# Performance work log

Hardware: AMD Instinct MI355X
Metric: run time of the kernel (lower is better)

## Reference

```python
import jax, jax.numpy as jnp
import numpy as np

N = 100000      # nodes
E = 1600000     # edges (avg degree 16)
F_IN = 300      # input feature dim
H = 64          # hidden channels
OUT = 20        # output classes
L = 8           # num GCN2Conv layers
ALPHA = 0.1
THETA = 0.5


def setup_inputs() -> dict:
    key = jax.random.key(0)
    ks = jax.random.split(key, 6)
    x = jax.random.normal(ks[0], (N, F_IN), jnp.float32)
    edge_index = jax.random.randint(ks[1], (2, E), 0, N, dtype=jnp.int32)
    edge_weights = jax.random.uniform(ks[2], (E,), jnp.float32)
    W_in = jax.random.normal(ks[3], (F_IN, H), jnp.float32) / np.sqrt(F_IN)
    b_in = jnp.zeros((H,), jnp.float32)
    conv_w = jax.random.normal(ks[4], (L, H, H), jnp.float32) / np.sqrt(H)
    W_out = jax.random.normal(ks[5], (H, OUT), jnp.float32) / np.sqrt(H)
    b_out = jnp.zeros((OUT,), jnp.float32)
    return dict(x=x, edge_index=edge_index, edge_weights=edge_weights,
                W_in=W_in, b_in=b_in, conv_w=conv_w, W_out=W_out, b_out=b_out)


def _gcn_norm(edge_index, edge_weights, n, dtype):
    # add self-loops with weight 1, symmetric normalization (PyG gcn_norm)
    loop = jnp.arange(n, dtype=edge_index.dtype)
    row = jnp.concatenate([edge_index[0], loop])
    col = jnp.concatenate([edge_index[1], loop])
    w = jnp.concatenate([edge_weights, jnp.ones((n,), dtype)])
    deg = jax.ops.segment_sum(w, col, num_segments=n)
    dinv = jnp.where(deg > 0, jax.lax.rsqrt(deg), 0.0).astype(dtype)
    norm = dinv[row] * w * dinv[col]
    return row, col, norm


def reference(x, edge_index, edge_weights, W_in, b_in, conv_w, W_out, b_out):
    n = x.shape[0]
    row, col, norm = _gcn_norm(edge_index, edge_weights, n, x.dtype)
    # eval mode: dropout is identity
    h = jax.nn.relu(x @ W_in + b_in)   # start_with_lin (F_IN != H)
    x0 = h
    num_layers = conv_w.shape[0]
    for l in range(num_layers):
        beta = float(np.log(THETA / (l + 1) + 1.0))
        # A_hat @ h : gather sources, weight by norm, scatter-add to targets
        agg = jax.ops.segment_sum(norm[:, None] * h[row], col, num_segments=n)
        z = (1.0 - ALPHA) * agg + ALPHA * x0  # initial-residual mixing
        h = jax.nn.relu((1.0 - beta) * z + beta * (z @ conv_w[l]))
    return h @ W_out + b_out
```

## Files before the change

kernel.cpp:

```cpp
#include <hip/hip_runtime.h>
#include <hip/hip_fp16.h>
#include <math.h>


#define HID 64
#define FIN 300
#define NOUT 20
#define ALPHA 0.1f
#define DSCALE 262144.0f
#define CNT_SHIFT 25
#define DEG_MASK 0x1FFFFFFu
#define FBLK 1024

typedef _Float16 f16;
typedef f16 f16x8 __attribute__((ext_vector_type(8)));
typedef float f32x4 __attribute__((ext_vector_type(4)));

__device__ __forceinline__ float wdec(unsigned v) {
    union { unsigned short u; __half h; } c;
    c.u = (unsigned short)(v >> 17);
    return __half2float(c.h);
}

__device__ __forceinline__ void unpack8(const float4& v, float* f) {
    const __half2* p = reinterpret_cast<const __half2*>(&v);
#pragma unroll
    for (int i = 0; i < 4; ++i) {
        float2 t = __half22float2(p[i]);
        f[2 * i] = t.x;
        f[2 * i + 1] = t.y;
    }
}

__global__ void accum_k(const int* __restrict__ row, const int* __restrict__ col,
                        const float* __restrict__ ew,
                        unsigned* __restrict__ packed,
                        uint2* __restrict__ rec, int e) {
    int i = blockIdx.x * blockDim.x + threadIdx.x;
    if (i < e) {
        int c = col[i], r = row[i];
        float wv = ew[i];
        unsigned q = (unsigned)__float2uint_rn(wv * DSCALE);
        unsigned old = atomicAdd(&packed[c], (1u << CNT_SHIFT) | q);
        unsigned rank = (old >> CNT_SHIFT) & 0x7Fu;
        union { __half h; unsigned short u; } cv;
        cv.h = __float2half(wv);
        rec[i] = make_uint2((unsigned)c | (rank << 17),
                            (unsigned)r | ((unsigned)cv.u << 17));
    }
}

__global__ __launch_bounds__(1024) void unpackscan_k(const unsigned* __restrict__ packed,
                                                     float* __restrict__ dinv,
                                                     int* __restrict__ padcnt,
                                                     int* __restrict__ bsum, int n) {
    __shared__ int ws[16];
    int t = threadIdx.x, i = blockIdx.x * 1024 + t;
    int pad = 0;
    if (i < n) {
        unsigned v = packed[i];
        int cnt = (int)(v >> CNT_SHIFT);
        float d = 1.0f + (float)(v & DEG_MASK) * (1.0f / DSCALE);
        dinv[i] = rsqrtf(d);
        pad = (cnt + 3) & ~3;
        padcnt[i] = pad;
    }
    int s = pad;
#pragma unroll
    for (int d = 1; d < 64; d <<= 1) s += __shfl_xor(s, d);
    if ((t & 63) == 0) ws[t >> 6] = s;
    __syncthreads();
    if (t == 0) {
        int tot = 0;
#pragma unroll
        for (int k = 0; k < 16; ++k) tot += ws[k];
        bsum[blockIdx.x] = tot;
    }
}

__global__ void scan2_k(int* __restrict__ bsum, int nb, int* __restrict__ rp, int n) {
    int lane = threadIdx.x;
    int acc = 0;
    for (int base = 0; base < nb; base += 64) {
        int idx = base + lane;
        int orig = (idx < nb) ? bsum[idx] : 0;
        int v = orig;
#pragma unroll
        for (int d = 1; d < 64; d <<= 1) {
            int u = __shfl_up(v, d);
            if (lane >= d) v += u;
        }
        if (idx < nb) bsum[idx] = acc + v - orig;
        acc += __shfl(v, 63);
    }
    if (lane == 0) rp[n] = acc;
}

__global__ __launch_bounds__(1024) void scan3_k(const int* __restrict__ padcnt,
                                                const unsigned* __restrict__ packed,
                                                const int* __restrict__ bsum,
                                                int* __restrict__ rp,
                                                unsigned* __restrict__ edges, int n) {
    __shared__ int ws[16];
    int t = threadIdx.x, i = blockIdx.x * 1024 + t;
    int lane = t & 63, w = t >> 6;
    int v = (i < n) ? padcnt[i] : 0;
    int sv = v;
#pragma unroll
    for (int d = 1; d < 64; d <<= 1) {
        int u = __shfl_up(sv, d);
        if (lane >= d) sv += u;
    }
    if (lane == 63) ws[w] = sv;
    __syncthreads();
    if (w == 0) {
        int x = (lane < 16) ? ws[lane] : 0;
#pragma unroll
        for (int d = 1; d < 16; d <<= 1) {
            int u = __shfl_up(x, d);
            if (lane >= d) x += u;
        }
        if (lane < 16) ws[lane] = x;
    }
    __syncthreads();
    int woff = (w > 0) ? ws[w - 1] : 0;
    if (i < n) {
        int base = bsum[blockIdx.x] + woff + sv - v;
        rp[i] = base;
        int cnt = (int)(packed[i] >> CNT_SHIFT);
        for (int k = cnt; k < v; ++k) edges[base + k] = 0u;
    }
}

__global__ void wt_k(const float* __restrict__ Win, f16* __restrict__ Wt) {
    int i = blockIdx.x * blockDim.x + threadIdx.x;
    if (i < 64 * 320) {
        int c = i / 320, k = i - c * 320;
        Wt[i] = (k < FIN) ? (f16)Win[k * 64 + c] : (f16)0.0f;
    }
}

__global__ __launch_bounds__(256) void fgi_k(const uint2* __restrict__ rec,
                                             const float* __restrict__ dinv,
                                             const int* __restrict__ rp,
                                             unsigned* __restrict__ edges, int e,
                                             const float* __restrict__ x,
                                             const f16* __restrict__ Wt,
                                             const float* __restrict__ bin,
                                             __half* __restrict__ x0h, int n) {
    __shared__ f16 As[64 * 72];
    int t = threadIdx.x;
    if (blockIdx.x < FBLK) {
        int xcd = blockIdx.x & 7;
        int lo = (int)(((long long)n * xcd) >> 3);
        int hi = (int)(((long long)n * (xcd + 1)) >> 3);
        int stride = (FBLK >> 3) * 256;
        for (int i = (blockIdx.x >> 3) * 256 + t; i < e; i += stride) {
            uint2 rc = rec[i];
            int c = (int)(rc.x & 0x1FFFFu);
            if (c < lo || c >= hi) continue;
            int r = (int)(rc.y & 0x1FFFFu);
            union { unsigned short u; __half h; } ev;
            ev.u = (unsigned short)(rc.y >> 17);
            float nw = (1.0f - ALPHA) * dinv[r] * __half2float(ev.h) * dinv[c];
            union { __half h; unsigned short u; } cv;
            cv.h = __float2half(nw);
            int rank = (int)((rc.x >> 17) & 0x7Fu);
            edges[rp[c] + rank] = ((unsigned)cv.u << 17) | (unsigned)r;
        }
        return;
    }
    int lane = t & 63, wv = t >> 6;
    int node0 = (blockIdx.x - FBLK) * 64;
    int lr = lane & 15, kg = lane >> 4;
    int fi = t & 15, rowbase = t >> 4;
    f32x4 acc0 = {0, 0, 0, 0}, acc1 = {0, 0, 0, 0}, acc2 = {0, 0, 0, 0}, acc3 = {0, 0, 0, 0};
    float4 xr[4];
    auto loadchunk = [&](int c) {
#pragma unroll
        for (int it = 0; it < 4; ++it) {
            int rw = rowbase + it * 16;
            int rr = node0 + rw;
            rr = (rr < n) ? rr : (n - 1);
            int kbase = c * 64 + fi * 4;
            xr[it] = make_float4(0.f, 0.f, 0.f, 0.f);
            if (kbase < FIN)
                xr[it] = *reinterpret_cast<const float4*>(x + (size_t)rr * FIN + kbase);
        }
    };
    loadchunk(0);
    for (int c = 0; c < 5; ++c) {
        __syncthreads();
#pragma unroll
        for (int it = 0; it < 4; ++it) {
            int rw = rowbase + it * 16;
            union { float2 f2; f16 h[4]; } u;
            u.h[0] = (f16)xr[it].x; u.h[1] = (f16)xr[it].y;
            u.h[2] = (f16)xr[it].z; u.h[3] = (f16)xr[it].w;
            *reinterpret_cast<float2*>(As + rw * 72 + fi * 4) = u.f2;
        }
        __syncthreads();
        if (c < 4) loadchunk(c + 1);
#pragma unroll
        for (int ks = 0; ks < 2; ++ks) {
            f16x8 a = *(const f16x8*)(As + (wv * 16 + lr) * 72 + ks * 32 + kg * 8);
            const f16* wb = Wt + c * 64 + ks * 32 + kg * 8;
            f16x8 b0 = *(const f16x8*)(wb + (0 * 16 + lr) * 320);
            f16x8 b1 = *(const f16x8*)(wb + (1 * 16 + lr) * 320);
            f16x8 b2 = *(const f16x8*)(wb + (2 * 16 + lr) * 320);
            f16x8 b3 = *(const f16x8*)(wb + (3 * 16 + lr) * 320);
            acc0 = __builtin_amdgcn_mfma_f32_16x16x32_f16(a, b0, acc0, 0, 0, 0);
            acc1 = __builtin_amdgcn_mfma_f32_16x16x32_f16(a, b1, acc1, 0, 0, 0);
            acc2 = __builtin_amdgcn_mfma_f32_16x16x32_f16(a, b2, acc2, 0, 0, 0);
            acc3 = __builtin_amdgcn_mfma_f32_16x16x32_f16(a, b3, acc3, 0, 0, 0);
        }
    }
    float bi0 = bin[0 * 16 + lr], bi1 = bin[1 * 16 + lr];
    float bi2 = bin[2 * 16 + lr], bi3 = bin[3 * 16 + lr];
    f16 ov[4][4];
#pragma unroll
    for (int r = 0; r < 4; ++r) {
        ov[0][r] = (f16)fmaxf(acc0[r] + bi0, 0.f);
        ov[1][r] = (f16)fmaxf(acc1[r] + bi1, 0.f);
        ov[2][r] = (f16)fmaxf(acc2[r] + bi2, 0.f);
        ov[3][r] = (f16)fmaxf(acc3[r] + bi3, 0.f);
    }
    __syncthreads();
#pragma unroll
    for (int cg = 0; cg < 4; ++cg)
#pragma unroll
        for (int r = 0; r < 4; ++r)
            As[(wv * 16 + kg * 4 + r) * 72 + cg * 16 + lr] = ov[cg][r];
    __syncthreads();
#pragma unroll
    for (int it = 0; it < 2; ++it) {
        int idx = t + it * 256;
        int rw = idx >> 3, ch = idx & 7;
        int node = node0 + rw;
        if (node < n)
            ((float4*)(x0h + (size_t)node * 64))[ch] =
                *reinterpret_cast<const float4*>(As + rw * 72 + ch * 8);
    }
}

__global__ __launch_bounds__(256) void layer_k(const int* __restrict__ rp,
                                               const unsigned* __restrict__ edges,
                                               const float* __restrict__ dinv,
                                               const __half* __restrict__ x0h,
                                               const __half* __restrict__ hin,
                                               __half* __restrict__ hout,
                                               const float* __restrict__ Wl,
                                               float beta, int n,
                                               const float* __restrict__ Wout,
                                               const float* __restrict__ bout,
                                               float* __restrict__ out) {
    __shared__ f16 As[64 * 72];
    __shared__ f16 Bs[64 * 72];
    int t = threadIdx.x, lane = t & 63, wv = t >> 6;
    int node0 = blockIdx.x * 64;
    for (int i = t; i < 4096; i += 256) {
        int k = i >> 6, c = i & 63;
        Bs[c * 72 + k] = (f16)Wl[i];
    }
    int g = lane >> 3, c8 = lane & 7;
#pragma unroll
    for (int pass = 0; pass < 2; ++pass) {
        int row = pass * 32 + wv * 8 + g;
        int node = node0 + row;
        int nd = (node < n) ? node : (n - 1);
        int j = rp[nd], end = (node < n) ? rp[nd + 1] : j;
        float a0[8], a1[8], a2[8], a3[8];
#pragma unroll
        for (int i = 0; i < 8; ++i) { a0[i] = 0.f; a1[i] = 0.f; a2[i] = 0.f; a3[i] = 0.f; }
        while (__any(j < end)) {
            if (j < end) {
                uint4 e4 = *reinterpret_cast<const uint4*>(edges + j);
                float w0 = wdec(e4.x), w1 = wdec(e4.y), w2 = wdec(e4.z), w3 = wdec(e4.w);
                float4 r0 = ((const float4*)(hin + (size_t)(e4.x & 0x1FFFF) * 64))[c8];
                float4 r1 = ((const float4*)(hin + (size_t)(e4.y & 0x1FFFF) * 64))[c8];
                float4 r2 = ((const float4*)(hin + (size_t)(e4.z & 0x1FFFF) * 64))[c8];
                float4 r3 = ((const float4*)(hin + (size_t)(e4.w & 0x1FFFF) * 64))[c8];
                float f0[8], f1[8], f2[8], f3[8];
                unpack8(r0, f0);
                unpack8(r1, f1);
                unpack8(r2, f2);
                unpack8(r3, f3);
#pragma unroll
                for (int i = 0; i < 8; ++i) {
                    a0[i] = fmaf(w0, f0[i], a0[i]);
                    a1[i] = fmaf(w1, f1[i], a1[i]);
                    a2[i] = fmaf(w2, f2[i], a2[i]);
                    a3[i] = fmaf(w3, f3[i], a3[i]);
                }
            }
            j += 4;
        }
        float di = dinv[nd];
        float c1 = (1.0f - ALPHA) * di * di;
        float4 hs4 = ((const float4*)(hin + (size_t)nd * 64))[c8];
        float4 xs4 = ((const float4*)(x0h + (size_t)nd * 64))[c8];
        float hf[8], xf[8];
        unpack8(hs4, hf);
        unpack8(xs4, xf);
        f16x8 zv8;
#pragma unroll
        for (int i = 0; i < 8; ++i)
            zv8[i] = (f16)fmaf(ALPHA, xf[i],
                               fmaf(c1, hf[i], (a0[i] + a1[i]) + (a2[i] + a3[i])));
        *(f16x8*)(As + row * 72 + c8 * 8) = zv8;
    }
    __syncthreads();
    int lr = lane & 15, kg = lane >> 4;
    f32x4 acc0 = {0, 0, 0, 0}, acc1 = {0, 0, 0, 0}, acc2 = {0, 0, 0, 0}, acc3 = {0, 0, 0, 0};
    f16x8 af0 = *(const f16x8*)(As + (wv * 16 + lr) * 72 + kg * 8);
    f16x8 af1 = *(const f16x8*)(As + (wv * 16 + lr) * 72 + 32 + kg * 8);
    {
        f16x8 b0 = *(const f16x8*)(Bs + (0 * 16 + lr) * 72 + kg * 8);
        f16x8 b1 = *(const f16x8*)(Bs + (0 * 16 + lr) * 72 + 32 + kg * 8);
        acc0 = __builtin_amdgcn_mfma_f32_16x16x32_f16(af0, b0, acc0, 0, 0, 0);
        acc0 = __builtin_amdgcn_mfma_f32_16x16x32_f16(af1, b1, acc0, 0, 0, 0);
    }
    {
        f16x8 b0 = *(const f16x8*)(Bs + (1 * 16 + lr) * 72 + kg * 8);
        f16x8 b1 = *(const f16x8*)(Bs + (1 * 16 + lr) * 72 + 32 + kg * 8);
        acc1 = __builtin_amdgcn_mfma_f32_16x16x32_f16(af0, b0, acc1, 0, 0, 0);
        acc1 = __builtin_amdgcn_mfma_f32_16x16x32_f16(af1, b1, acc1, 0, 0, 0);
    }
    {
        f16x8 b0 = *(const f16x8*)(Bs + (2 * 16 + lr) * 72 + kg * 8);
        f16x8 b1 = *(const f16x8*)(Bs + (2 * 16 + lr) * 72 + 32 + kg * 8);
        acc2 = __builtin_amdgcn_mfma_f32_16x16x32_f16(af0, b0, acc2, 0, 0, 0);
        acc2 = __builtin_amdgcn_mfma_f32_16x16x32_f16(af1, b1, acc2, 0, 0, 0);
    }
    {
        f16x8 b0 = *(const f16x8*)(Bs + (3 * 16 + lr) * 72 + kg * 8);
        f16x8 b1 = *(const f16x8*)(Bs + (3 * 16 + lr) * 72 + 32 + kg * 8);
        acc3 = __builtin_amdgcn_mfma_f32_16x16x32_f16(af0, b0, acc3, 0, 0, 0);
        acc3 = __builtin_amdgcn_mfma_f32_16x16x32_f16(af1, b1, acc3, 0, 0, 0);
    }
    float omb = 1.0f - beta;
    f16 ov[4][4];
#pragma unroll
    for (int cg = 0; cg < 4; ++cg) {
        f32x4 acc = (cg == 0) ? acc0 : (cg == 1) ? acc1 : (cg == 2) ? acc2 : acc3;
        int col = cg * 16 + lr;
#pragma unroll
        for (int r = 0; r < 4; ++r) {
            float zv = (float)As[(wv * 16 + kg * 4 + r) * 72 + col];
            ov[cg][r] = (f16)fmaxf(fmaf(beta, acc[r], omb * zv), 0.f);
        }
    }
    __syncthreads();
#pragma unroll
    for (int cg = 0; cg < 4; ++cg)
#pragma unroll
        for (int r = 0; r < 4; ++r)
            As[(wv * 16 + kg * 4 + r) * 72 + cg * 16 + lr] = ov[cg][r];
    __syncthreads();

    if (!Wout) {
#pragma unroll
        for (int it = 0; it < 2; ++it) {
            int idx = t + it * 256;
            int rw = idx >> 3, ch = idx & 7;
            int node = node0 + rw;
            if (node < n)
                ((float4*)(hout + (size_t)node * 64))[ch] =
                    *reinterpret_cast<const float4*>(As + rw * 72 + ch * 8);
        }
    } else {
        for (int i = t; i < 32 * 64; i += 256) {
            int c = i >> 6, k = i & 63;
            Bs[c * 72 + k] = (c < NOUT) ? (f16)Wout[k * NOUT + c] : (f16)0.0f;
        }
        __syncthreads();
        f16x8 ha0 = *(const f16x8*)(As + (wv * 16 + lr) * 72 + kg * 8);
        f16x8 ha1 = *(const f16x8*)(As + (wv * 16 + lr) * 72 + 32 + kg * 8);
#pragma unroll
        for (int ct = 0; ct < 2; ++ct) {
            f32x4 oacc = {0, 0, 0, 0};
            f16x8 b0 = *(const f16x8*)(Bs + (ct * 16 + lr) * 72 + kg * 8);
            f16x8 b1 = *(const f16x8*)(Bs + (ct * 16 + lr) * 72 + 32 + kg * 8);
            oacc = __builtin_amdgcn_mfma_f32_16x16x32_f16(ha0, b0, oacc, 0, 0, 0);
            oacc = __builtin_amdgcn_mfma_f32_16x16x32_f16(ha1, b1, oacc, 0, 0, 0);
            int col = ct * 16 + lr;
            if (col < NOUT) {
                float bo = bout[col];
#pragma unroll
                for (int r = 0; r < 4; ++r) {
                    int nd2 = node0 + wv * 16 + kg * 4 + r;
                    if (nd2 < n) out[(size_t)nd2 * NOUT + col] = oacc[r] + bo;
                }
            }
        }
    }
}

extern "C" void kernel_launch(void* const* d_in, const int* in_sizes, int n_in,
                              void* d_out, int out_size, void* d_ws, size_t ws_size,
                              hipStream_t stream) {
    const float* x    = (const float*)d_in[0];
    const int*   ei   = (const int*)d_in[1];
    const float* ew   = (const float*)d_in[2];
    const float* Win  = (const float*)d_in[3];
    const float* bin  = (const float*)d_in[4];
    const float* cw   = (const float*)d_in[5];
    const float* Wout = (const float*)d_in[6];
    const float* bout = (const float*)d_in[7];

    const int n = in_sizes[0] / FIN;
    const int e = in_sizes[2];
    const int L = in_sizes[5] / (HID * HID);
    const int* row = ei;
    const int* col = ei + e;
    const int epadmax = e + 3 * n + 64;

    size_t off = 0;
    auto alloc = [&](size_t bytes) -> char* {
        char* q = (char*)d_ws + off;
        off = (off + bytes + 255) & ~(size_t)255;
        return q;
    };
    __half* x0h  = (__half*)alloc((size_t)n * HID * 2);
    __half* hA   = (__half*)alloc((size_t)n * HID * 2);
    __half* hB   = (__half*)alloc((size_t)n * HID * 2);
    unsigned* edges = (unsigned*)alloc((size_t)epadmax * 4);
    uint2* rec   = (uint2*)alloc((size_t)e * 8);
    unsigned* packed = (unsigned*)alloc((size_t)n * 4);
    float* dinv  = (float*)alloc((size_t)n * 4);
    int*   padcnt= (int*)alloc((size_t)n * 4);
    int*   rp    = (int*)alloc((size_t)(n + 1) * 4);
    int*   bsum  = (int*)alloc(1024 * 4);
    f16*   Wt    = (f16*)alloc((size_t)64 * 320 * 2);

    const int nb = (n + 1023) / 1024;
    const int ntile = (n + 63) / 64;

    hipMemsetAsync(packed, 0, (size_t)n * 4, stream);
    wt_k<<<(64 * 320 + 255) / 256, 256, 0, stream>>>(Win, Wt);
    accum_k<<<(e + 255) / 256, 256, 0, stream>>>(row, col, ew, packed, rec, e);
    unpackscan_k<<<nb, 1024, 0, stream>>>(packed, dinv, padcnt, bsum, n);
    scan2_k<<<1, 64, 0, stream>>>(bsum, nb, rp, n);
    scan3_k<<<nb, 1024, 0, stream>>>(padcnt, packed, bsum, rp, edges, n);

    fgi_k<<<FBLK + ntile, 256, 0, stream>>>(rec, dinv, rp, edges, e,
                                            x, Wt, bin, x0h, n);

    const __half* hin = x0h;
    __half* hout = hA;
    for (int l = 0; l < L; ++l) {
        float beta = (float)log(0.5 / (double)(l + 1) + 1.0);
        bool last = (l == L - 1);
        layer_k<<<ntile, 256, 0, stream>>>(rp, edges, dinv, x0h, hin, hout,
                                           cw + (size_t)l * HID * HID, beta, n,
                                           last ? Wout : nullptr,
                                           last ? bout : nullptr,
                                           last ? (float*)d_out : nullptr);
        hin = hout;
        hout = (hout == hA) ? hB : hA;
    }
}
```

Before: 481.5 us.

## Dynamically assign node rows to 8-lane groups via shared work queue

Replaces the fixed two-pass row assignment in the layer kernel with a dynamic queue: each 8-lane group takes a row, and when it finishes it grabs the next row index from a shared-memory atomic counter. This targets load imbalance from varying node degrees, where a wave used to stall until its longest row finished. In exchange the loop carries extra control flow, a shared atomic and shuffle per iteration, plus an added block barrier.

```diff
diff --git a/kernel.cpp b/kernel.cpp
--- a/kernel.cpp
+++ b/kernel.cpp
@@ -256,58 +256,81 @@
                                                float* __restrict__ out) {
     __shared__ f16 As[64 * 72];
     __shared__ f16 Bs[64 * 72];
+    __shared__ int qctr;
     int t = threadIdx.x, lane = t & 63, wv = t >> 6;
     int node0 = blockIdx.x * 64;
+    if (t == 0) qctr = 32;
     for (int i = t; i < 4096; i += 256) {
         int k = i >> 6, c = i & 63;
         Bs[c * 72 + k] = (f16)Wl[i];
     }
-    int g = lane >> 3, c8 = lane & 7;
-#pragma unroll
-    for (int pass = 0; pass < 2; ++pass) {
-        int row = pass * 32 + wv * 8 + g;
-        int node = node0 + row;
-        int nd = (node < n) ? node : (n - 1);
-        int j = rp[nd], end = (node < n) ? rp[nd + 1] : j;
-        float a0[8], a1[8], a2[8], a3[8];
+    int c8 = lane & 7;
+    __syncthreads();
+
+    int myrow = t >> 3;
+    int nd = 0, j = 0, end = 0;
+    float a0[8], a1[8], a2[8], a3[8];
+    {
+        int node = node0 + myrow;
+        nd = (node < n) ? node : (n - 1);
+        j = rp[nd];
+        end = (node < n) ? rp[nd + 1] : j;
 #pragma unroll
         for (int i = 0; i < 8; ++i) { a0[i] = 0.f; a1[i] = 0.f; a2[i] = 0.f; a3[i] = 0.f; }
-        while (__any(j < end)) {
-            if (j < end) {
-                uint4 e4 = *reinterpret_cast<const uint4*>(edges + j);
-                float w0 = wdec(e4.x), w1 = wdec(e4.y), w2 = wdec(e4.z), w3 = wdec(e4.w);
-                float4 r0 = ((const float4*)(hin + (size_t)(e4.x & 0x1FFFF) * 64))[c8];
-                float4 r1 = ((const float4*)(hin + (size_t)(e4.y & 0x1FFFF) * 64))[c8];
-                float4 r2 = ((const float4*)(hin + (size_t)(e4.z & 0x1FFFF) * 64))[c8];
-                float4 r3 = ((const float4*)(hin + (size_t)(e4.w & 0x1FFFF) * 64))[c8];
-                float f0[8], f1[8], f2[8], f3[8];
-                unpack8(r0, f0);
-                unpack8(r1, f1);
-                unpack8(r2, f2);
-                unpack8(r3, f3);
-#pragma unroll
-                for (int i = 0; i < 8; ++i) {
-                    a0[i] = fmaf(w0, f0[i], a0[i]);
-                    a1[i] = fmaf(w1, f1[i], a1[i]);
-                    a2[i] = fmaf(w2, f2[i], a2[i]);
-                    a3[i] = fmaf(w3, f3[i], a3[i]);
-                }
+    }
+    for (;;) {
+        bool fin = (myrow >= 0) && (j >= end);
+        if (fin) {
+            float di = dinv[nd];
+            float c1 = (1.0f - ALPHA) * di * di;
+            float4 hs4 = ((const float4*)(hin + (size_t)nd * 64))[c8];
+            float4 xs4 = ((const float4*)(x0h + (size_t)nd * 64))[c8];
+            float hf[8], xf[8];
+            unpack8(hs4, hf);
+            unpack8(xs4, xf);
+            f16x8 zv8;
+#pragma unroll
+            for (int i = 0; i < 8; ++i)
+                zv8[i] = (f16)fmaf(ALPHA, xf[i],
+                                   fmaf(c1, hf[i], (a0[i] + a1[i]) + (a2[i] + a3[i])));
+            *(f16x8*)(As + myrow * 72 + c8 * 8) = zv8;
+        }
+        int newrow = 1 << 30;
+        if (fin && c8 == 0) newrow = atomicAdd(&qctr, 1);
+        newrow = __shfl(newrow, lane & 56);
+        if (fin) {
+            myrow = (newrow < 64) ? newrow : -1;
+            if (myrow >= 0) {
+                int node = node0 + myrow;
+                nd = (node < n) ? node : (n - 1);
+                j = rp[nd];
+                end = (node < n) ? rp[nd + 1] : j;
+#pragma unroll
+                for (int i = 0; i < 8; ++i) { a0[i] = 0.f; a1[i] = 0.f; a2[i] = 0.f; a3[i] = 0.f; }
+            }
+        }
+        if (!__any(myrow >= 0)) break;
+        if (myrow >= 0 && j < end) {
+            uint4 e4 = *reinterpret_cast<const uint4*>(edges + j);
+            float w0 = wdec(e4.x), w1 = wdec(e4.y), w2 = wdec(e4.z), w3 = wdec(e4.w);
+            float4 r0 = ((const float4*)(hin + (size_t)(e4.x & 0x1FFFF) * 64))[c8];
+            float4 r1 = ((const float4*)(hin + (size_t)(e4.y & 0x1FFFF) * 64))[c8];
+            float4 r2 = ((const float4*)(hin + (size_t)(e4.z & 0x1FFFF) * 64))[c8];
+            float4 r3 = ((const float4*)(hin + (size_t)(e4.w & 0x1FFFF) * 64))[c8];
+            float f0[8], f1[8], f2[8], f3[8];
+            unpack8(r0, f0);
+            unpack8(r1, f1);
+            unpack8(r2, f2);
+            unpack8(r3, f3);
+#pragma unroll
+            for (int i = 0; i < 8; ++i) {
+                a0[i] = fmaf(w0, f0[i], a0[i]);
+                a1[i] = fmaf(w1, f1[i], a1[i]);
+                a2[i] = fmaf(w2, f2[i], a2[i]);
+                a3[i] = fmaf(w3, f3[i], a3[i]);
             }
             j += 4;
         }
-        float di = dinv[nd];
-        float c1 = (1.0f - ALPHA) * di * di;
-        float4 hs4 = ((const float4*)(hin + (size_t)nd * 64))[c8];
-        float4 xs4 = ((const float4*)(x0h + (size_t)nd * 64))[c8];
-        float hf[8], xf[8];
-        unpack8(hs4, hf);
-        unpack8(xs4, xf);
-        f16x8 zv8;
-#pragma unroll
-        for (int i = 0; i < 8; ++i)
-            zv8[i] = (f16)fmaf(ALPHA, xf[i],
-                               fmaf(c1, hf[i], (a0[i] + a1[i]) + (a2[i] + a3[i])));
-        *(f16x8*)(As + row * 72 + c8 * 8) = zv8;
     }
     __syncthreads();
     int lr = lane & 15, kg = lane >> 4;
```

Result: slower. 543.9 us (+13.0%).

## Split fused edge-fill/input-GEMM kernel and double-buffer input feature loads

Applied to the files above, without the earlier changes.

Splits the combined kernel, where one set of blocks filled the CSR edge array and another set computed the input projection GEMM, into two separate kernels launched back to back. The input GEMM now prefetches two chunks of x ahead using two register buffers, where before it held one. The intent is to stop the edge-fill blocks and the GEMM blocks from competing for the same launch, and to hide more of the global-memory latency of the x reads. In exchange, the two phases can no longer overlap, there is one extra kernel launch, and the GEMM uses more registers.

```diff
diff --git a/kernel.cpp b/kernel.cpp
--- a/kernel.cpp
+++ b/kernel.cpp
@@ -10,7 +10,6 @@
 #define DSCALE 262144.0f
 #define CNT_SHIFT 25
 #define DEG_MASK 0x1FFFFFFu
-#define FBLK 1024
 
 typedef _Float16 f16;
 typedef f16 f16x8 __attribute__((ext_vector_type(8)));
@@ -132,6 +131,31 @@
     }
 }
 
+__global__ __launch_bounds__(256) void fill_k(const uint2* __restrict__ rec,
+                                              const float* __restrict__ dinv,
+                                              const int* __restrict__ rp,
+                                              unsigned* __restrict__ edges,
+                                              int e, int n) {
+    int xcd = blockIdx.x & 7;
+    int lo = (int)(((long long)n * xcd) >> 3);
+    int hi = (int)(((long long)n * (xcd + 1)) >> 3);
+    int nblk = gridDim.x >> 3;
+    int stride = nblk * 256;
+    for (int i = (blockIdx.x >> 3) * 256 + threadIdx.x; i < e; i += stride) {
+        uint2 rc = rec[i];
+        int c = (int)(rc.x & 0x1FFFFu);
+        if (c < lo || c >= hi) continue;
+        int r = (int)(rc.y & 0x1FFFFu);
+        union { unsigned short u; __half h; } ev;
+        ev.u = (unsigned short)(rc.y >> 17);
+        float nw = (1.0f - ALPHA) * dinv[r] * __half2float(ev.h) * dinv[c];
+        union { __half h; unsigned short u; } cv;
+        cv.h = __float2half(nw);
+        int rank = (int)((rc.x >> 17) & 0x7Fu);
+        edges[rp[c] + rank] = ((unsigned)cv.u << 17) | (unsigned)r;
+    }
+}
+
 __global__ void wt_k(const float* __restrict__ Win, f16* __restrict__ Wt) {
     int i = blockIdx.x * blockDim.x + threadIdx.x;
     if (i < 64 * 320) {
@@ -140,81 +164,75 @@
     }
 }
 
-__global__ __launch_bounds__(256) void fgi_k(const uint2* __restrict__ rec,
-                                             const float* __restrict__ dinv,
-                                             const int* __restrict__ rp,
-                                             unsigned* __restrict__ edges, int e,
-                                             const float* __restrict__ x,
-                                             const f16* __restrict__ Wt,
-                                             const float* __restrict__ bin,
-                                             __half* __restrict__ x0h, int n) {
+__global__ __launch_bounds__(256) void gemm_in_k(const float* __restrict__ x,
+                                                 const f16* __restrict__ Wt,
+                                                 const float* __restrict__ bin,
+                                                 __half* __restrict__ x0h, int n) {
     __shared__ f16 As[64 * 72];
-    int t = threadIdx.x;
-    if (blockIdx.x < FBLK) {
-        int xcd = blockIdx.x & 7;
-        int lo = (int)(((long long)n * xcd) >> 3);
-        int hi = (int)(((long long)n * (xcd + 1)) >> 3);
-        int stride = (FBLK >> 3) * 256;
-        for (int i = (blockIdx.x >> 3) * 256 + t; i < e; i += stride) {
-            uint2 rc = rec[i];
-            int c = (int)(rc.x & 0x1FFFFu);
-            if (c < lo || c >= hi) continue;
-            int r = (int)(rc.y & 0x1FFFFu);
-            union { unsigned short u; __half h; } ev;
-            ev.u = (unsigned short)(rc.y >> 17);
-            float nw = (1.0f - ALPHA) * dinv[r] * __half2float(ev.h) * dinv[c];
-            union { __half h; unsigned short u; } cv;
-            cv.h = __float2half(nw);
-            int rank = (int)((rc.x >> 17) & 0x7Fu);
-            edges[rp[c] + rank] = ((unsigned)cv.u << 17) | (unsigned)r;
-        }
-        return;
-    }
-    int lane = t & 63, wv = t >> 6;
-    int node0 = (blockIdx.x - FBLK) * 64;
+    int t = threadIdx.x, lane = t & 63, wv = t >> 6;
+    int node0 = blockIdx.x * 64;
     int lr = lane & 15, kg = lane >> 4;
     int fi = t & 15, rowbase = t >> 4;
     f32x4 acc0 = {0, 0, 0, 0}, acc1 = {0, 0, 0, 0}, acc2 = {0, 0, 0, 0}, acc3 = {0, 0, 0, 0};
-    float4 xr[4];
-    auto loadchunk = [&](int c) {
-#pragma unroll
-        for (int it = 0; it < 4; ++it) {
-            int rw = rowbase + it * 16;
-            int rr = node0 + rw;
-            rr = (rr < n) ? rr : (n - 1);
-            int kbase = c * 64 + fi * 4;
-            xr[it] = make_float4(0.f, 0.f, 0.f, 0.f);
-            if (kbase < FIN)
-                xr[it] = *reinterpret_cast<const float4*>(x + (size_t)rr * FIN + kbase);
-        }
-    };
-    loadchunk(0);
-    for (int c = 0; c < 5; ++c) {
-        __syncthreads();
-#pragma unroll
-        for (int it = 0; it < 4; ++it) {
-            int rw = rowbase + it * 16;
-            union { float2 f2; f16 h[4]; } u;
-            u.h[0] = (f16)xr[it].x; u.h[1] = (f16)xr[it].y;
-            u.h[2] = (f16)xr[it].z; u.h[3] = (f16)xr[it].w;
-            *reinterpret_cast<float2*>(As + rw * 72 + fi * 4) = u.f2;
-        }
-        __syncthreads();
-        if (c < 4) loadchunk(c + 1);
-#pragma unroll
-        for (int ks = 0; ks < 2; ++ks) {
-            f16x8 a = *(const f16x8*)(As + (wv * 16 + lr) * 72 + ks * 32 + kg * 8);
-            const f16* wb = Wt + c * 64 + ks * 32 + kg * 8;
-            f16x8 b0 = *(const f16x8*)(wb + (0 * 16 + lr) * 320);
-            f16x8 b1 = *(const f16x8*)(wb + (1 * 16 + lr) * 320);
-            f16x8 b2 = *(const f16x8*)(wb + (2 * 16 + lr) * 320);
-            f16x8 b3 = *(const f16x8*)(wb + (3 * 16 + lr) * 320);
-            acc0 = __builtin_amdgcn_mfma_f32_16x16x32_f16(a, b0, acc0, 0, 0, 0);
-            acc1 = __builtin_amdgcn_mfma_f32_16x16x32_f16(a, b1, acc1, 0, 0, 0);
-            acc2 = __builtin_amdgcn_mfma_f32_16x16x32_f16(a, b2, acc2, 0, 0, 0);
-            acc3 = __builtin_amdgcn_mfma_f32_16x16x32_f16(a, b3, acc3, 0, 0, 0);
-        }
-    }
+    float4 xrA[4], xrB[4];
+
+#define LOADCHUNK(buf, c)                                                       \
+    {                                                                           \
+        _Pragma("unroll")                                                       \
+        for (int it = 0; it < 4; ++it) {                                        \
+            int rw = rowbase + it * 16;                                         \
+            int rr = node0 + rw;                                                \
+            rr = (rr < n) ? rr : (n - 1);                                       \
+            int kbase = (c) * 64 + fi * 4;                                      \
+            buf[it] = make_float4(0.f, 0.f, 0.f, 0.f);                          \
+            if (kbase < FIN)                                                    \
+                buf[it] = *reinterpret_cast<const float4*>(                     \
+                    x + (size_t)rr * FIN + kbase);                              \
+        }                                                                       \
+    }
+
+#define STAGE(buf)                                                              \
+    {                                                                           \
+        __syncthreads();                                                        \
+        _Pragma("unroll")                                                       \
+        for (int it = 0; it < 4; ++it) {                                        \
+            int rw = rowbase + it * 16;                                         \
+            union { float2 f2; f16 h[4]; } u;                                   \
+            u.h[0] = (f16)buf[it].x; u.h[1] = (f16)buf[it].y;                   \
+            u.h[2] = (f16)buf[it].z; u.h[3] = (f16)buf[it].w;                   \
+            *reinterpret_cast<float2*>(As + rw * 72 + fi * 4) = u.f2;           \
+        }                                                                       \
+        __syncthreads();                                                        \
+    }
+
+#define DOMFMA(c)                                                               \
+    {                                                                           \
+        _Pragma("unroll")                                                       \
+        for (int ks = 0; ks < 2; ++ks) {                                        \
+            f16x8 a = *(const f16x8*)(As + (wv * 16 + lr) * 72 + ks * 32 + kg * 8); \
+            const f16* wb = Wt + (c) * 64 + ks * 32 + kg * 8;                   \
+            f16x8 b0 = *(const f16x8*)(wb + (0 * 16 + lr) * 320);               \
+            f16x8 b1 = *(const f16x8*)(wb + (1 * 16 + lr) * 320);               \
+            f16x8 b2 = *(const f16x8*)(wb + (2 * 16 + lr) * 320);               \
+            f16x8 b3 = *(const f16x8*)(wb + (3 * 16 + lr) * 320);               \
+            acc0 = __builtin_amdgcn_mfma_f32_16x16x32_f16(a, b0, acc0, 0, 0, 0); \
+            acc1 = __builtin_amdgcn_mfma_f32_16x16x32_f16(a, b1, acc1, 0, 0, 0); \
+            acc2 = __builtin_amdgcn_mfma_f32_16x16x32_f16(a, b2, acc2, 0, 0, 0); \
+            acc3 = __builtin_amdgcn_mfma_f32_16x16x32_f16(a, b3, acc3, 0, 0, 0); \
+        }                                                                       \
+    }
+
+    LOADCHUNK(xrA, 0);
+    LOADCHUNK(xrB, 1);
+    STAGE(xrA); LOADCHUNK(xrA, 2); DOMFMA(0);
+    STAGE(xrB); LOADCHUNK(xrB, 3); DOMFMA(1);
+    STAGE(xrA); LOADCHUNK(xrA, 4); DOMFMA(2);
+    STAGE(xrB); DOMFMA(3);
+    STAGE(xrA); DOMFMA(4);
+#undef LOADCHUNK
+#undef STAGE
+#undef DOMFMA
+
     float bi0 = bin[0 * 16 + lr], bi1 = bin[1 * 16 + lr];
     float bi2 = bin[2 * 16 + lr], bi3 = bin[3 * 16 + lr];
     f16 ov[4][4];
@@ -442,9 +460,8 @@
     unpackscan_k<<<nb, 1024, 0, stream>>>(packed, dinv, padcnt, bsum, n);
     scan2_k<<<1, 64, 0, stream>>>(bsum, nb, rp, n);
     scan3_k<<<nb, 1024, 0, stream>>>(padcnt, packed, bsum, rp, edges, n);
-
-    fgi_k<<<FBLK + ntile, 256, 0, stream>>>(rec, dinv, rp, edges, e,
-                                            x, Wt, bin, x0h, n);
+    fill_k<<<1024, 256, 0, stream>>>(rec, dinv, rp, edges, e, n);
+    gemm_in_k<<<ntile, 256, 0, stream>>>(x, Wt, bin, x0h, n);
 
     const __half* hin = x0h;
     __half* hout = hA;
```

Result: no change. 489.5 us (+1.7%).

## Privatize degree/count atomics into eight copies to cut atomic contention

Applied to the files above, without the earlier changes.

The per-node atomic counter that accumulates degree and edge rank is replicated into eight copies selected by block index, and each edge record now stores which copy it used. The unpack kernel sums the copies and stores per-copy byte offsets, and the scatter adds that offset to the rank. The intent is to spread atomics across memory and reduce same-address contention on the atomic path. In exchange it adds a larger memset, an extra read pass over eight arrays, and a new kernel that zeroes the padding slots.

```diff
diff --git a/kernel.cpp b/kernel.cpp
--- a/kernel.cpp
+++ b/kernel.cpp
@@ -34,35 +34,46 @@
 
 __global__ void accum_k(const int* __restrict__ row, const int* __restrict__ col,
                         const float* __restrict__ ew,
-                        unsigned* __restrict__ packed,
-                        uint2* __restrict__ rec, int e) {
+                        unsigned* __restrict__ packed8,
+                        uint2* __restrict__ rec, int e, int n) {
     int i = blockIdx.x * blockDim.x + threadIdx.x;
     if (i < e) {
+        int copy = blockIdx.x & 7;
         int c = col[i], r = row[i];
         float wv = ew[i];
         unsigned q = (unsigned)__float2uint_rn(wv * DSCALE);
-        unsigned old = atomicAdd(&packed[c], (1u << CNT_SHIFT) | q);
+        unsigned old = atomicAdd(&packed8[(size_t)copy * n + c],
+                                 (1u << CNT_SHIFT) | q);
         unsigned rank = (old >> CNT_SHIFT) & 0x7Fu;
         union { __half h; unsigned short u; } cv;
         cv.h = __float2half(wv);
-        rec[i] = make_uint2((unsigned)c | (rank << 17),
+        rec[i] = make_uint2((unsigned)c | ((unsigned)copy << 17) | (rank << 20),
                             (unsigned)r | ((unsigned)cv.u << 17));
     }
 }
 
-__global__ __launch_bounds__(1024) void unpackscan_k(const unsigned* __restrict__ packed,
+__global__ __launch_bounds__(1024) void unpackscan_k(const unsigned* __restrict__ packed8,
                                                      float* __restrict__ dinv,
+                                                     unsigned char* __restrict__ off8,
                                                      int* __restrict__ padcnt,
                                                      int* __restrict__ bsum, int n) {
     __shared__ int ws[16];
     int t = threadIdx.x, i = blockIdx.x * 1024 + t;
     int pad = 0;
     if (i < n) {
-        unsigned v = packed[i];
-        int cnt = (int)(v >> CNT_SHIFT);
-        float d = 1.0f + (float)(v & DEG_MASK) * (1.0f / DSCALE);
+        unsigned cnt = 0, dsum = 0;
+        union { unsigned char b[8]; uint2 u2; } offs;
+#pragma unroll
+        for (int k = 0; k < 8; ++k) {
+            unsigned v = packed8[(size_t)k * n + i];
+            offs.b[k] = (unsigned char)cnt;
+            cnt += (v >> CNT_SHIFT);
+            dsum += (v & DEG_MASK);
+        }
+        float d = 1.0f + (float)dsum * (1.0f / DSCALE);
         dinv[i] = rsqrtf(d);
-        pad = (cnt + 3) & ~3;
+        reinterpret_cast<uint2*>(off8)[i] = offs.u2;
+        pad = (int)((cnt + 3u) & ~3u);
         padcnt[i] = pad;
     }
     int s = pad;
@@ -97,7 +108,6 @@
 }
 
 __global__ __launch_bounds__(1024) void scan3_k(const int* __restrict__ padcnt,
-                                                const unsigned* __restrict__ packed,
                                                 const int* __restrict__ bsum,
                                                 int* __restrict__ rp,
                                                 unsigned* __restrict__ edges, int n) {
@@ -127,8 +137,6 @@
     if (i < n) {
         int base = bsum[blockIdx.x] + woff + sv - v;
         rp[i] = base;
-        int cnt = (int)(packed[i] >> CNT_SHIFT);
-        for (int k = cnt; k < v; ++k) edges[base + k] = 0u;
     }
 }
 
@@ -140,9 +148,23 @@
     }
 }
 
+__global__ void padzero_k(const int* __restrict__ rp, const int* __restrict__ padcnt,
+                          const unsigned char* __restrict__ off8,
+                          const unsigned* __restrict__ packed8,
+                          unsigned* __restrict__ edges, int n) {
+    int i = blockIdx.x * blockDim.x + threadIdx.x;
+    if (i >= n) return;
+    unsigned c7 = packed8[(size_t)7 * n + i] >> CNT_SHIFT;
+    int truecnt = (int)off8[i * 8 + 7] + (int)c7;
+    int pad = padcnt[i];
+    int base = rp[i];
+    for (int k = truecnt; k < pad; ++k) edges[base + k] = 0u;
+}
+
 __global__ __launch_bounds__(256) void fgi_k(const uint2* __restrict__ rec,
                                              const float* __restrict__ dinv,
                                              const int* __restrict__ rp,
+                                             const unsigned char* __restrict__ off8,
                                              unsigned* __restrict__ edges, int e,
                                              const float* __restrict__ x,
                                              const f16* __restrict__ Wt,
@@ -165,8 +187,10 @@
             float nw = (1.0f - ALPHA) * dinv[r] * __half2float(ev.h) * dinv[c];
             union { __half h; unsigned short u; } cv;
             cv.h = __float2half(nw);
-            int rank = (int)((rc.x >> 17) & 0x7Fu);
-            edges[rp[c] + rank] = ((unsigned)cv.u << 17) | (unsigned)r;
+            int copy = (int)((rc.x >> 17) & 7u);
+            int rank = (int)((rc.x >> 20) & 0x7Fu);
+            edges[rp[c] + (int)off8[c * 8 + copy] + rank] =
+                ((unsigned)cv.u << 17) | (unsigned)r;
         }
         return;
     }
@@ -426,7 +450,8 @@
     __half* hB   = (__half*)alloc((size_t)n * HID * 2);
     unsigned* edges = (unsigned*)alloc((size_t)epadmax * 4);
     uint2* rec   = (uint2*)alloc((size_t)e * 8);
-    unsigned* packed = (unsigned*)alloc((size_t)n * 4);
+    unsigned* packed8 = (unsigned*)alloc((size_t)8 * n * 4);
+    unsigned char* off8 = (unsigned char*)alloc((size_t)n * 8);
     float* dinv  = (float*)alloc((size_t)n * 4);
     int*   padcnt= (int*)alloc((size_t)n * 4);
     int*   rp    = (int*)alloc((size_t)(n + 1) * 4);
@@ -436,14 +461,15 @@
     const int nb = (n + 1023) / 1024;
     const int ntile = (n + 63) / 64;
 
-    hipMemsetAsync(packed, 0, (size_t)n * 4, stream);
+    hipMemsetAsync(packed8, 0, (size_t)8 * n * 4, stream);
     wt_k<<<(64 * 320 + 255) / 256, 256, 0, stream>>>(Win, Wt);
-    accum_k<<<(e + 255) / 256, 256, 0, stream>>>(row, col, ew, packed, rec, e);
-    unpackscan_k<<<nb, 1024, 0, stream>>>(packed, dinv, padcnt, bsum, n);
+    accum_k<<<(e + 255) / 256, 256, 0, stream>>>(row, col, ew, packed8, rec, e, n);
+    unpackscan_k<<<nb, 1024, 0, stream>>>(packed8, dinv, off8, padcnt, bsum, n);
     scan2_k<<<1, 64, 0, stream>>>(bsum, nb, rp, n);
-    scan3_k<<<nb, 1024, 0, stream>>>(padcnt, packed, bsum, rp, edges, n);
-
-    fgi_k<<<FBLK + ntile, 256, 0, stream>>>(rec, dinv, rp, edges, e,
+    scan3_k<<<nb, 1024, 0, stream>>>(padcnt, bsum, rp, edges, n);
+    padzero_k<<<(n + 255) / 256, 256, 0, stream>>>(rp, padcnt, off8, packed8, edges, n);
+
+    fgi_k<<<FBLK + ntile, 256, 0, stream>>>(rec, dinv, rp, off8, edges, e,
                                             x, Wt, bin, x0h, n);
 
     const __half* hin = x0h;
```

After: 481.8 us. Within noise of the previous version (+0.1%).
